# Kernel tuning notes

Measured on AMD Instinct MI355X. Metric: run time of the kernel, lower is better.

The kernel has to match this reference:

```python
import jax, jax.numpy as jnp
import numpy as np

NUM_GROUPS = 8
INPUT_DIM = 1024
OUTPUT_DIM = 1024
TOKENS_PER_GROUP = 8192  # rows per group after reshape


def setup_inputs() -> dict:
    key = jax.random.key(0)
    kx, kw = jax.random.split(key)
    # x: [N*G, D_in] as fed to the torch module (it reshapes internally)
    x = jax.random.normal(kx, (TOKENS_PER_GROUP * NUM_GROUPS, INPUT_DIM), dtype=jnp.float32)
    # Stacked per-group Linear weights, torch layout [D_out, D_in] per group.
    # Xavier-normal gain=1: std = sqrt(2 / (fan_in + fan_out))
    std = np.sqrt(2.0 / (INPUT_DIM + OUTPUT_DIM)).astype(np.float32)
    W = jax.random.normal(kw, (NUM_GROUPS, OUTPUT_DIM, INPUT_DIM), dtype=jnp.float32) * std
    return {"x": x, "W": W}


def reference(x, W):
    # x: [N*G, D_in] -> [N, G, D_in]
    n = x.shape[0] // NUM_GROUPS
    xg = x.reshape(n, NUM_GROUPS, INPUT_DIM)
    # per-group linear: out[n,g,k] = sum_d xg[n,g,d] * W[g,k,d]
    out = jnp.einsum("ngd,gkd->ngk", xg, W)
    return out.reshape(-1, OUTPUT_DIM)
```

## Files before the change

### kernel.cpp

```cpp
#include <hip/hip_runtime.h>
#include <hip/hip_bf16.h>


namespace {

constexpr int NG   = 8;
constexpr int DIN  = 1024;
constexpr int DOUT = 1024;
constexpr int BM   = 128;
constexpr int BN   = 256;
constexpr int BK   = 32;
constexpr int NKT  = DIN / BK;
constexpr int ROWB  = BK * 2;
constexpr int ATILE = BM * ROWB;
constexpr int BTILE = BN * ROWB;
constexpr int JTN  = DOUT / BN;
constexpr size_t WSB_BYTES = (size_t)NG * JTN * NKT * BTILE;

typedef __attribute__((ext_vector_type(8))) short bf16x8;
typedef __attribute__((ext_vector_type(4))) float f32x4;

__device__ __forceinline__ bf16x8 pack_bf16x8v(f32x4 lo, f32x4 hi) {
  union { __hip_bfloat162 h2[4]; bf16x8 v; } p;
  p.h2[0] = __float22bfloat162_rn(make_float2(lo.x, lo.y));
  p.h2[1] = __float22bfloat162_rn(make_float2(lo.z, lo.w));
  p.h2[2] = __float22bfloat162_rn(make_float2(hi.x, hi.y));
  p.h2[3] = __float22bfloat162_rn(make_float2(hi.z, hi.w));
  return p.v;
}

__device__ __forceinline__ void glds16(const void* g, void* l) {
  __builtin_amdgcn_global_load_lds(
      (const __attribute__((address_space(1))) unsigned int*)g,
      (__attribute__((address_space(3))) unsigned int*)l, 16, 0, 0);
}

#define FENCE() asm volatile("" ::: "memory")
#define BAR()   do { FENCE(); __builtin_amdgcn_s_barrier(); FENCE(); } while (0)
#define LGKM0() asm volatile("s_waitcnt lgkmcnt(0)" ::: "memory")
#define VM0()   asm volatile("s_waitcnt vmcnt(0)" ::: "memory")
#define VMC2()  asm volatile("s_waitcnt vmcnt(2)" ::: "memory")
#define MFMA_(a, b, c) __builtin_amdgcn_mfma_f32_16x16x32_bf16((a), (b), (c), 0, 0, 0)

__global__ __launch_bounds__(256)
void cvt_w_kernel(const float* __restrict__ W, char* __restrict__ wsB) {
  const int q    = (int)blockIdx.x * 256 + (int)threadIdx.x;
  const int tile = q >> 10;
  const int qi   = q & 1023;
  const int r    = qi >> 2;
  const int w    = qi & 3;
  const int g    = tile >> 7;
  const int jt   = (tile >> 5) & 3;
  const int kt   = tile & 31;

  const float* src = W + (size_t)(g * DOUT + jt * BN + r) * DIN
                       + kt * BK + ((w ^ ((r >> 1) & 3)) * 8);
  f32x4 lo = *(const f32x4*)(src);
  f32x4 hi = *(const f32x4*)(src + 4);
  *(bf16x8*)(wsB + (size_t)q * 16) = pack_bf16x8v(lo, hi);
}

#define KBODY(T, CUR)                                                          \
  {                                                                            \
    const int t_ = (T);                                                        \
    char* const cA = smA + (CUR) * ATILE;                                      \
    char* const cB = smB + (CUR) * BTILE;                                      \
    char* const nA = smA + (1 - (CUR)) * ATILE;                                \
    char* const nB = smB + (1 - (CUR)) * BTILE;                                \
    const bool st1 = (t_ + 1) < NKT;                                           \
    const bool st2 = (t_ + 2) < NKT;                                           \
    if (WSB) {                                                                 \
      if (st1) {        \
        const char* Bn = BgT + (size_t)(t_ + 1) * BTILE;                       \
        glds16(Bn + tid * 16, nB + tid * 16);                                  \
        glds16(Bn + 8192 + tid * 16, nB + 8192 + tid * 16);                    \
      }                                                                        \
      FENCE();                                                                 \
    }                                                                          \
    if (st2) {                         \
      const float* An = aSrc + (size_t)(t_ + 2) * BK;                          \
      aS[CUR][0] = *(const f32x4*)(An);                                        \
      aS[CUR][1] = *(const f32x4*)(An + 4);                                    \
    }                                                                          \
    if (!WSB && st1) {                                                         \
      const float* Bn = bSrc + (size_t)(t_ + 1) * BK;                          \
      bS[0] = *(const f32x4*)(Bn);                                             \
      bS[1] = *(const f32x4*)(Bn + 4);                                         \
      bS[2] = *(const f32x4*)(Bn + (size_t)128 * DIN);                         \
      bS[3] = *(const f32x4*)(Bn + (size_t)128 * DIN + 4);                     \
    }                                                                          \
    FENCE();                                                                   \
    bf16x8 bfr[4];                                                             \
    _Pragma("unroll")                                                          \
    for (int n = 0; n < 4; ++n)                                                \
      bfr[n] = *(const bf16x8*)(cB + boff + n * 1024);                         \
    __builtin_amdgcn_s_setprio(1);                                             \
    _Pragma("unroll")                                                          \
    for (int m = 0; m < 4; ++m) {                                              \
      bf16x8 am = *(const bf16x8*)(cA + aoff + m * 1024);                      \
      _Pragma("unroll")                                                        \
      for (int n = 0; n < 4; ++n)                                              \
        acc[m][n] = MFMA_(am, bfr[n], acc[m][n]);                              \
    }                                                                          \
    __builtin_amdgcn_s_setprio(0);                                             \
    if (st1) {                                                                 \
       \
      *(bf16x8*)(nA + tid * 16) = pack_bf16x8v(aS[1 - (CUR)][0],               \
                                               aS[1 - (CUR)][1]);              \
      if (!WSB) {                                                              \
        *(bf16x8*)(nB + tid * 16)        = pack_bf16x8v(bS[0], bS[1]);         \
        *(bf16x8*)(nB + tid * 16 + 8192) = pack_bf16x8v(bS[2], bS[3]);         \
      }                                                                        \
      LGKM0();                                                                 \
      if (WSB) { if (st2) { VMC2(); } else { VM0(); } }                        \
      BAR();                                                                   \
    }                                                                          \
  }

template <bool WSB>
__global__ __launch_bounds__(512, 4)
void gemm_k(const float* __restrict__ X, const float* __restrict__ W,
            const char* __restrict__ wsB, float* __restrict__ O) {
  __shared__ __align__(16) char smA[2 * ATILE];
  __shared__ __align__(16) char smB[2 * BTILE];

  const int bid = (int)blockIdx.x;
  const int swz = (bid & 7) * 256 + (bid >> 3);
  const int jt = swz & 3;
  const int it = (swz >> 2) & 63;
  const int g  = swz >> 8;

  const int n0 = it * BM;
  const int c0 = jt * BN;

  const int tid  = (int)threadIdx.x;
  const int lane = tid & 63;
  const int wid  = tid >> 6;
  const int wr   = wid >> 2;
  const int wc   = wid & 3;
  const int fr   = lane & 15;
  const int fq   = lane >> 4;

  {
  }
  const int aRow = tid >> 2;
  const int aChk = (tid & 3) ^ ((tid >> 3) & 3);
  const float* aSrc = X + ((size_t)(n0 + aRow) * NG + g) * DIN + aChk * 8;

  const char* BgT = wsB + (size_t)((g * JTN + jt) * NKT) * BTILE;
  const int bRow = tid >> 2;
  const int bChk = (tid & 3) ^ ((tid >> 3) & 3);
  const float* bSrc = W + (size_t)(g * DOUT + c0 + bRow) * DIN + bChk * 8;

  const int psw  = (fq ^ ((fr >> 1) & 3)) << 4;
  const int aoff = (wr * 64 + fr) * ROWB + psw;
  const int boff = (wc * 64 + fr) * ROWB + psw;

  f32x4 aS[2][2];
  f32x4 bS[4];
  f32x4 acc[4][4];
#pragma unroll
  for (int m = 0; m < 4; ++m)
#pragma unroll
    for (int n = 0; n < 4; ++n) acc[m][n] = (f32x4){0.f, 0.f, 0.f, 0.f};

  aS[0][0] = *(const f32x4*)(aSrc);
  aS[0][1] = *(const f32x4*)(aSrc + 4);
  if (WSB) {
    glds16(BgT + tid * 16, smB + tid * 16);
    glds16(BgT + 8192 + tid * 16, smB + 8192 + tid * 16);
  } else {
    bS[0] = *(const f32x4*)(bSrc);
    bS[1] = *(const f32x4*)(bSrc + 4);
    bS[2] = *(const f32x4*)(bSrc + (size_t)128 * DIN);
    bS[3] = *(const f32x4*)(bSrc + (size_t)128 * DIN + 4);
  }
  FENCE();
  aS[1][0] = *(const f32x4*)(aSrc + BK);
  aS[1][1] = *(const f32x4*)(aSrc + BK + 4);
  FENCE();
  *(bf16x8*)(smA + tid * 16) = pack_bf16x8v(aS[0][0], aS[0][1]);
  if (!WSB) {
    *(bf16x8*)(smB + tid * 16)        = pack_bf16x8v(bS[0], bS[1]);
    *(bf16x8*)(smB + tid * 16 + 8192) = pack_bf16x8v(bS[2], bS[3]);
  }
  LGKM0();
  if (WSB) { VMC2(); }
  BAR();

  for (int tt = 0; tt < NKT; tt += 2) {
    KBODY(tt, 0);
    KBODY(tt + 1, 1);
  }

#pragma unroll
  for (int m = 0; m < 4; ++m) {
#pragma unroll
    for (int r = 0; r < 4; ++r) {
      const int row = wr * 64 + m * 16 + fq * 4 + r;
      float* orow = O + ((size_t)(n0 + row) * NG + g) * DOUT + c0 + wc * 64;
#pragma unroll
      for (int n = 0; n < 4; ++n) {
        orow[n * 16 + fr] = acc[m][n][r];
      }
    }
  }
}

}

extern "C" void kernel_launch(void* const* d_in, const int* in_sizes, int n_in,
                              void* d_out, int out_size, void* d_ws, size_t ws_size,
                              hipStream_t stream) {
  (void)n_in; (void)out_size;
  const float* X = (const float*)d_in[0];
  const float* W = (const float*)d_in[1];
  float* O = (float*)d_out;

  const int tokens_total = in_sizes[0] / DIN;
  const int ntok_per_g   = tokens_total / NG;
  const int grid = NG * (ntok_per_g / BM) * (DOUT / BN);

  if (ws_size >= WSB_BYTES) {
    const int cvt_grid = (int)(WSB_BYTES / 16 / 256);
    cvt_w_kernel<<<dim3(cvt_grid), dim3(256), 0, stream>>>(W, (char*)d_ws);
    gemm_k<true><<<dim3(grid), dim3(512), 0, stream>>>(
        X, W, (const char*)d_ws, O);
  } else {
    gemm_k<false><<<dim3(grid), dim3(512), 0, stream>>>(
        X, W, nullptr, O);
  }
}
```

Before: 230.5 us.

## Load B fragments directly from pre-swizzled global layout into registers, dropping B LDS

The weight conversion kernel now writes bf16 weights in MFMA fragment order, so each wave can load its B operand fragments straight from global memory into registers. The B shared-memory tiles, the async global-to-LDS copies and their vmcnt waits are removed, which cuts LDS traffic and footprint. In exchange, each wave re-reads B from global/L2 with no sharing across the two waves that use the same columns. The B load for the next k-step is also issued after the MFMAs with only one register buffer, so load latency may be exposed.

Measured after the change: 236.8 us. +2.7%, slower.

```diff
diff --git a/kernel.cpp b/kernel.cpp
--- a/kernel.cpp
+++ b/kernel.cpp
@@ -13,9 +13,9 @@
 constexpr int NKT  = DIN / BK;
 constexpr int ROWB  = BK * 2;
 constexpr int ATILE = BM * ROWB;
-constexpr int BTILE = BN * ROWB;
 constexpr int JTN  = DOUT / BN;
-constexpr size_t WSB_BYTES = (size_t)NG * JTN * NKT * BTILE;
+constexpr int FRAGT = 16 * 1024;
+constexpr size_t WSB_BYTES = (size_t)NG * JTN * NKT * FRAGT;
 
 typedef __attribute__((ext_vector_type(8))) short bf16x8;
 typedef __attribute__((ext_vector_type(4))) float f32x4;
@@ -29,32 +29,24 @@
   return p.v;
 }
 
-__device__ __forceinline__ void glds16(const void* g, void* l) {
-  __builtin_amdgcn_global_load_lds(
-      (const __attribute__((address_space(1))) unsigned int*)g,
-      (__attribute__((address_space(3))) unsigned int*)l, 16, 0, 0);
-}
-
 #define FENCE() asm volatile("" ::: "memory")
 #define BAR()   do { FENCE(); __builtin_amdgcn_s_barrier(); FENCE(); } while (0)
 #define LGKM0() asm volatile("s_waitcnt lgkmcnt(0)" ::: "memory")
-#define VM0()   asm volatile("s_waitcnt vmcnt(0)" ::: "memory")
-#define VMC2()  asm volatile("s_waitcnt vmcnt(2)" ::: "memory")
 #define MFMA_(a, b, c) __builtin_amdgcn_mfma_f32_16x16x32_bf16((a), (b), (c), 0, 0, 0)
 
 __global__ __launch_bounds__(256)
 void cvt_w_kernel(const float* __restrict__ W, char* __restrict__ wsB) {
   const int q    = (int)blockIdx.x * 256 + (int)threadIdx.x;
   const int tile = q >> 10;
-  const int qi   = q & 1023;
-  const int r    = qi >> 2;
-  const int w    = qi & 3;
+  const int f    = (q >> 6) & 15;
+  const int l    = q & 63;
   const int g    = tile >> 7;
   const int jt   = (tile >> 5) & 3;
   const int kt   = tile & 31;
 
-  const float* src = W + (size_t)(g * DOUT + jt * BN + r) * DIN
-                       + kt * BK + ((w ^ ((r >> 1) & 3)) * 8);
+  const int row = jt * BN + (f >> 2) * 64 + (f & 3) * 16 + (l & 15);
+  const int col = kt * BK + (l >> 4) * 8;
+  const float* src = W + (size_t)(g * DOUT + row) * DIN + col;
   f32x4 lo = *(const f32x4*)(src);
   f32x4 hi = *(const f32x4*)(src + 4);
   *(bf16x8*)(wsB + (size_t)q * 16) = pack_bf16x8v(lo, hi);
@@ -64,55 +56,40 @@
   {                                                                            \
     const int t_ = (T);                                                        \
     char* const cA = smA + (CUR) * ATILE;                                      \
-    char* const cB = smB + (CUR) * BTILE;                                      \
     char* const nA = smA + (1 - (CUR)) * ATILE;                                \
-    char* const nB = smB + (1 - (CUR)) * BTILE;                                \
     const bool st1 = (t_ + 1) < NKT;                                           \
     const bool st2 = (t_ + 2) < NKT;                                           \
-    if (WSB) {                                                                 \
-      if (st1) {        \
-        const char* Bn = BgT + (size_t)(t_ + 1) * BTILE;                       \
-        glds16(Bn + tid * 16, nB + tid * 16);                                  \
-        glds16(Bn + 8192 + tid * 16, nB + 8192 + tid * 16);                    \
-      }                                                                        \
-      FENCE();                                                                 \
-    }                                                                          \
-    if (st2) {                         \
+    if (st2) {                  \
       const float* An = aSrc + (size_t)(t_ + 2) * BK;                          \
       aS[CUR][0] = *(const f32x4*)(An);                                        \
       aS[CUR][1] = *(const f32x4*)(An + 4);                                    \
     }                                                                          \
-    if (!WSB && st1) {                                                         \
-      const float* Bn = bSrc + (size_t)(t_ + 1) * BK;                          \
-      bS[0] = *(const f32x4*)(Bn);                                             \
-      bS[1] = *(const f32x4*)(Bn + 4);                                         \
-      bS[2] = *(const f32x4*)(Bn + (size_t)128 * DIN);                         \
-      bS[3] = *(const f32x4*)(Bn + (size_t)128 * DIN + 4);                     \
-    }                                                                          \
-    FENCE();                                                                   \
-    bf16x8 bfr[4];                                                             \
-    _Pragma("unroll")                                                          \
-    for (int n = 0; n < 4; ++n)                                                \
-      bfr[n] = *(const bf16x8*)(cB + boff + n * 1024);                         \
     __builtin_amdgcn_s_setprio(1);                                             \
     _Pragma("unroll")                                                          \
     for (int m = 0; m < 4; ++m) {                                              \
       bf16x8 am = *(const bf16x8*)(cA + aoff + m * 1024);                      \
       _Pragma("unroll")                                                        \
       for (int n = 0; n < 4; ++n)                                              \
-        acc[m][n] = MFMA_(am, bfr[n], acc[m][n]);                              \
+        acc[m][n] = MFMA_(am, bf[n], acc[m][n]);                               \
     }                                                                          \
     __builtin_amdgcn_s_setprio(0);                                             \
     if (st1) {                                                                 \
-       \
+      if (WSB) {        \
+        const char* Bn = BgF + (size_t)(t_ + 1) * FRAGT;                       \
+        _Pragma("unroll")                                                      \
+        for (int n = 0; n < 4; ++n)                                            \
+          bf[n] = *(const bf16x8*)(Bn + n * 1024);                             \
+      } else {                                                                 \
+        _Pragma("unroll")                                                      \
+        for (int n = 0; n < 4; ++n) {                                          \
+          const float* bp = bSrcF + (size_t)n * 16 * DIN + (t_ + 1) * BK;      \
+          bf[n] = pack_bf16x8v(*(const f32x4*)(bp), *(const f32x4*)(bp + 4));  \
+        }                                                                      \
+      }                                                                        \
+                   \
       *(bf16x8*)(nA + tid * 16) = pack_bf16x8v(aS[1 - (CUR)][0],               \
                                                aS[1 - (CUR)][1]);              \
-      if (!WSB) {                                                              \
-        *(bf16x8*)(nB + tid * 16)        = pack_bf16x8v(bS[0], bS[1]);         \
-        *(bf16x8*)(nB + tid * 16 + 8192) = pack_bf16x8v(bS[2], bS[3]);         \
-      }                                                                        \
       LGKM0();                                                                 \
-      if (WSB) { if (st2) { VMC2(); } else { VM0(); } }                        \
       BAR();                                                                   \
     }                                                                          \
   }
@@ -122,7 +99,6 @@
 void gemm_k(const float* __restrict__ X, const float* __restrict__ W,
             const char* __restrict__ wsB, float* __restrict__ O) {
   __shared__ __align__(16) char smA[2 * ATILE];
-  __shared__ __align__(16) char smB[2 * BTILE];
 
   const int bid = (int)blockIdx.x;
   const int swz = (bid & 7) * 256 + (bid >> 3);
@@ -141,23 +117,19 @@
   const int fr   = lane & 15;
   const int fq   = lane >> 4;
 
-  {
-  }
   const int aRow = tid >> 2;
   const int aChk = (tid & 3) ^ ((tid >> 3) & 3);
   const float* aSrc = X + ((size_t)(n0 + aRow) * NG + g) * DIN + aChk * 8;
 
-  const char* BgT = wsB + (size_t)((g * JTN + jt) * NKT) * BTILE;
-  const int bRow = tid >> 2;
-  const int bChk = (tid & 3) ^ ((tid >> 3) & 3);
-  const float* bSrc = W + (size_t)(g * DOUT + c0 + bRow) * DIN + bChk * 8;
-
-  const int psw  = (fq ^ ((fr >> 1) & 3)) << 4;
-  const int aoff = (wr * 64 + fr) * ROWB + psw;
-  const int boff = (wc * 64 + fr) * ROWB + psw;
+  const char* BgF = wsB + (size_t)((g * JTN + jt) * NKT) * FRAGT
+                        + (wc * 4) * 1024 + lane * 16;
+  const float* bSrcF = W + (size_t)(g * DOUT + c0 + wc * 64 + fr) * DIN
+                         + fq * 8;
+
+  const int aoff = (wr * 64 + fr) * ROWB + ((fq ^ ((fr >> 1) & 3)) << 4);
 
   f32x4 aS[2][2];
-  f32x4 bS[4];
+  bf16x8 bf[4];
   f32x4 acc[4][4];
 #pragma unroll
   for (int m = 0; m < 4; ++m)
@@ -167,25 +139,20 @@
   aS[0][0] = *(const f32x4*)(aSrc);
   aS[0][1] = *(const f32x4*)(aSrc + 4);
   if (WSB) {
-    glds16(BgT + tid * 16, smB + tid * 16);
-    glds16(BgT + 8192 + tid * 16, smB + 8192 + tid * 16);
+#pragma unroll
+    for (int n = 0; n < 4; ++n)
+      bf[n] = *(const bf16x8*)(BgF + n * 1024);
   } else {
-    bS[0] = *(const f32x4*)(bSrc);
-    bS[1] = *(const f32x4*)(bSrc + 4);
-    bS[2] = *(const f32x4*)(bSrc + (size_t)128 * DIN);
-    bS[3] = *(const f32x4*)(bSrc + (size_t)128 * DIN + 4);
-  }
-  FENCE();
+#pragma unroll
+    for (int n = 0; n < 4; ++n) {
+      const float* bp = bSrcF + (size_t)n * 16 * DIN;
+      bf[n] = pack_bf16x8v(*(const f32x4*)(bp), *(const f32x4*)(bp + 4));
+    }
+  }
   aS[1][0] = *(const f32x4*)(aSrc + BK);
   aS[1][1] = *(const f32x4*)(aSrc + BK + 4);
-  FENCE();
   *(bf16x8*)(smA + tid * 16) = pack_bf16x8v(aS[0][0], aS[0][1]);
-  if (!WSB) {
-    *(bf16x8*)(smB + tid * 16)        = pack_bf16x8v(bS[0], bS[1]);
-    *(bf16x8*)(smB + tid * 16 + 8192) = pack_bf16x8v(bS[2], bS[3]);
-  }
   LGKM0();
-  if (WSB) { VMC2(); }
   BAR();
 
   for (int tt = 0; tt < NKT; tt += 2) {
```
